# Kernel tuning notes

Hardware: AMD Instinct MI355X
Metric: run time of the kernel (lower is better)

## Reference

```python
import jax, jax.numpy as jnp
import numpy as np

MSA_DIM = 256
N_HEADS = 8
HEAD_DIM = MSA_DIM // N_HEADS
PAIR_DIM = 128
SCALE = 1.0 / float(np.sqrt(HEAD_DIM))


def setup_inputs() -> dict:
    key = jax.random.key(0)
    ks = jax.random.split(key, 7)
    B, S, L = 1, 128, 384
    return {
        "msa": jax.random.normal(ks[0], (B, S, L, MSA_DIM), dtype=jnp.float32),
        "pair": jax.random.normal(ks[1], (B, L, L, PAIR_DIM), dtype=jnp.float32),
        "Wq": jax.random.normal(ks[2], (MSA_DIM, MSA_DIM), dtype=jnp.float32) * 0.02,
        "Wk": jax.random.normal(ks[3], (MSA_DIM, MSA_DIM), dtype=jnp.float32) * 0.02,
        "Wv": jax.random.normal(ks[4], (MSA_DIM, MSA_DIM), dtype=jnp.float32) * 0.02,
        "Wo": jax.random.normal(ks[5], (MSA_DIM, MSA_DIM), dtype=jnp.float32) * 0.02,
        "Wpb": jax.random.normal(ks[6], (N_HEADS, PAIR_DIM), dtype=jnp.float32) * 0.02,
    }


def reference(msa, pair, Wq, Wk, Wv, Wo, Wpb):
    B, S, L, D = msa.shape
    H, hd = N_HEADS, HEAD_DIM
    # projections (nn.Linear: y = x @ W.T), split heads -> (B,S,H,L,hd)
    q = (msa @ Wq.T).reshape(B, S, L, H, hd)
    k = (msa @ Wk.T).reshape(B, S, L, H, hd)
    v = (msa @ Wv.T).reshape(B, S, L, H, hd)
    # NOTE: faithful to the original forward — pair_bias is computed but the
    # Triton kernel performs plain flash attention, so the bias is NOT added.
    _pair_bias = jnp.einsum('bijp,hp->bhij', pair, Wpb)  # dead code, as in source
    # attention logits per MSA row: (B,S,H,L,L)
    scores = jnp.einsum('bslhd,bsmhd->bshlm', q, k) * SCALE
    attn = jax.nn.softmax(scores, axis=-1)
    out = jnp.einsum('bshlm,bsmhd->bslhd', attn, v).reshape(B, S, L, D)
    return out @ Wo.T
```

## Files before the change

### kernel.cpp

```cpp
#include <hip/hip_runtime.h>
#include <stdint.h>

typedef unsigned short u16;
typedef __bf16 bf16x8 __attribute__((ext_vector_type(8)));
typedef short s16x4 __attribute__((ext_vector_type(4)));
typedef float f32x4 __attribute__((ext_vector_type(4)));

#define QKV_STRIDE 12288

__device__ __forceinline__ u16 f2bf(float x) {
    unsigned int u = __float_as_uint(x);
    u += 0x7fffu + ((u >> 16) & 1u);
    return (u16)(u >> 16);
}
__device__ __forceinline__ float bf2f(u16 h) {
    return __uint_as_float(((unsigned int)h) << 16);
}
__device__ __forceinline__ float tbf(float x) {
    return __uint_as_float(__float_as_uint(x) & 0xffff0000u);
}

static __device__ __forceinline__ f32x4 pv_mfma(s16x4 a, s16x4 b, f32x4 c) {
#if __has_builtin(__builtin_amdgcn_mfma_f32_16x16x16bf16_1k)
    return __builtin_amdgcn_mfma_f32_16x16x16bf16_1k(a, b, c, 0, 0, 0);
#else
    union { s16x4 h[2]; bf16x8 v; } ua, ub;
    s16x4 zz = {0, 0, 0, 0};
    ua.h[0] = a; ua.h[1] = zz;
    ub.h[0] = b; ub.h[1] = zz;
    return __builtin_amdgcn_mfma_f32_16x16x32_bf16(ua.v, ub.v, c, 0, 0, 0);
#endif
}

__global__ void convert_msa(const float* __restrict__ src, u16* __restrict__ dst) {
    int i = blockIdx.x * 256 + threadIdx.x;
    float4 v = ((const float4*)src)[i];
    ushort4 o;
    o.x = f2bf(v.x); o.y = f2bf(v.y); o.z = f2bf(v.z); o.w = f2bf(v.w);
    ((ushort4*)dst)[i] = o;
}

__global__ void pack_weights(const float* __restrict__ Wq, const float* __restrict__ Wk,
                             const float* __restrict__ Wv, const float* __restrict__ Wo,
                             u16* __restrict__ Wqkv, u16* __restrict__ Woh, u16* __restrict__ Wol) {
    int i = blockIdx.x * 256 + threadIdx.x;
    Wqkv[i]          = f2bf(Wq[i]);
    Wqkv[65536 + i]  = f2bf(Wk[i]);
    Wqkv[131072 + i] = f2bf(Wv[i]);
    float w = Wo[i];
    u16 hi = f2bf(w);
    Woh[i] = hi;
    Wol[i] = f2bf(w - bf2f(hi));
}

__launch_bounds__(256, 2)
__global__ void qkv_gemm(const u16* __restrict__ A, const u16* __restrict__ W,
                         u16* __restrict__ Qb, u16* __restrict__ Kb, u16* __restrict__ VTb) {
    __shared__ __align__(16) u16 As[128 * 32];
    __shared__ __align__(16) u16 Bs[128 * 32];
    const int tid = threadIdx.x;
    const int tm = blockIdx.x % 384, tn = blockIdx.x / 384;
    const bool trans = (tn < 4);
    const int lane = tid & 63, wave = tid >> 6;
    const int lm = lane & 15, lq = lane >> 4;
    const int wm = (wave >> 1) * 64, wn = (wave & 1) * 64;
    const float CEXPF = 0.17677669529663687f * 1.4426950408889634f;
    f32x4 acc[4][4] = {};

    const int ra = tid >> 2, ka = (tid & 3) << 3;
    const int rb = ra + 64;

    for (int k0 = 0; k0 < 256; k0 += 32) {
        *(uint4*)&As[ra * 32 + ka] = *(const uint4*)&A[(tm * 128 + ra) * 256 + k0 + ka];
        *(uint4*)&As[rb * 32 + ka] = *(const uint4*)&A[(tm * 128 + rb) * 256 + k0 + ka];
        *(uint4*)&Bs[ra * 32 + ka] = *(const uint4*)&W[(tn * 128 + ra) * 256 + k0 + ka];
        *(uint4*)&Bs[rb * 32 + ka] = *(const uint4*)&W[(tn * 128 + rb) * 256 + k0 + ka];
        __syncthreads();
        const u16* Xs = trans ? Bs : As;
        const u16* Ys = trans ? As : Bs;
        bf16x8 xf[4], yf[4];
        #pragma unroll
        for (int i = 0; i < 4; ++i)
            xf[i] = *(const bf16x8*)&Xs[(wm + i * 16 + lm) * 32 + lq * 8];
        #pragma unroll
        for (int j = 0; j < 4; ++j)
            yf[j] = *(const bf16x8*)&Ys[(wn + j * 16 + lm) * 32 + lq * 8];
        #pragma unroll
        for (int i = 0; i < 4; ++i)
            #pragma unroll
            for (int j = 0; j < 4; ++j)
                acc[i][j] = __builtin_amdgcn_mfma_f32_16x16x32_bf16(xf[i], yf[j], acc[i][j], 0, 0, 0);
        __syncthreads();
    }

    if (trans) {
        #pragma unroll
        for (int i = 0; i < 4; ++i) {
            int F0 = tn * 128 + wm + i * 16 + lq * 4;
            int which = F0 >> 8;
            int h = (F0 >> 5) & 7, d0 = F0 & 31;
            u16* dst = which ? Kb : Qb;
            float scale = which ? 1.0f : CEXPF;
            #pragma unroll
            for (int j = 0; j < 4; ++j) {
                int R = tm * 128 + wn + j * 16 + lm;
                int s = R / 384, l = R - s * 384;
                ushort4 o;
                o.x = f2bf(acc[i][j][0] * scale);
                o.y = f2bf(acc[i][j][1] * scale);
                o.z = f2bf(acc[i][j][2] * scale);
                o.w = f2bf(acc[i][j][3] * scale);
                *(ushort4*)&dst[((s * 8 + h) * 384 + l) * 32 + d0] = o;
            }
        }
    } else {
        #pragma unroll
        for (int j = 0; j < 4; ++j) {
            int F = tn * 128 + wn + j * 16 + lm;
            int h = (F >> 5) & 7, d = F & 31;
            #pragma unroll
            for (int i = 0; i < 4; ++i) {
                int R0 = tm * 128 + wm + i * 16 + lq * 4;
                int s = R0 / 384, l0 = R0 - s * 384;
                ushort4 o;
                o.x = f2bf(acc[i][j][0]);
                o.y = f2bf(acc[i][j][1]);
                o.z = f2bf(acc[i][j][2]);
                o.w = f2bf(acc[i][j][3]);
                *(ushort4*)&VTb[((s * 8 + h) * 32 + d) * 384 + l0] = o;
            }
        }
    }
}

__launch_bounds__(256, 3)
__global__ void msa_attention(const u16* __restrict__ Qb, const u16* __restrict__ Kb,
                              const u16* __restrict__ VTb,
                              u16* __restrict__ Ahi, u16* __restrict__ Alo) {
    __shared__ __align__(16) u16 Ks[384 * 32];
    __shared__ __align__(16) u16 Vt[32 * 392];
    const int tid = threadIdx.x;
    const int sh = blockIdx.x;
    const int s = sh >> 3, h = sh & 7;
    const u16* Qg = Qb + (size_t)sh * QKV_STRIDE;
    const u16* Kg = Kb + (size_t)sh * QKV_STRIDE;
    const u16* Vg = VTb + (size_t)sh * QKV_STRIDE;

    for (int i = tid; i < 1536; i += 256)
        *(uint4*)&Ks[i * 8] = *(const uint4*)&Kg[i * 8];
    for (int i = tid; i < 1536; i += 256) {
        int d = i / 48, c = i - d * 48;
        *(uint4*)&Vt[d * 392 + c * 8] = *(const uint4*)&Vg[d * 384 + c * 8];
    }

    const int lane = tid & 63, wave = tid >> 6;
    const int lm = lane & 15, lq = lane >> 4;

    bf16x8 aq[6];
    #pragma unroll
    for (int it = 0; it < 6; ++it)
        aq[it] = *(const bf16x8*)&Qg[((it * 4 + wave) * 16 + lm) * 32 + lq * 8];
    __syncthreads();

    f32x4 o[6][2] = {};
    float ls[6] = {0.f, 0.f, 0.f, 0.f, 0.f, 0.f};

    for (int n0 = 0; n0 < 384; n0 += 32) {
        bf16x8 kf0 = *(const bf16x8*)&Ks[(n0 + lm) * 32 + lq * 8];
        bf16x8 kf1 = *(const bf16x8*)&Ks[(n0 + 16 + lm) * 32 + lq * 8];
        s16x4 vf00 = *(const s16x4*)&Vt[lm * 392 + n0 + lq * 4];
        s16x4 vf01 = *(const s16x4*)&Vt[lm * 392 + n0 + 16 + lq * 4];
        s16x4 vf10 = *(const s16x4*)&Vt[(16 + lm) * 392 + n0 + lq * 4];
        s16x4 vf11 = *(const s16x4*)&Vt[(16 + lm) * 392 + n0 + 16 + lq * 4];
        #pragma unroll
        for (int it = 0; it < 6; ++it) {
            f32x4 z = {0.f, 0.f, 0.f, 0.f};
            f32x4 s0 = __builtin_amdgcn_mfma_f32_16x16x32_bf16(kf0, aq[it], z, 0, 0, 0);
            f32x4 s1 = __builtin_amdgcn_mfma_f32_16x16x32_bf16(kf1, aq[it], z, 0, 0, 0);
            float p0[4], p1[4];
            float a = 0.f;
            #pragma unroll
            for (int r = 0; r < 4; ++r) {
                p0[r] = __builtin_amdgcn_exp2f(s0[r]);
                p1[r] = __builtin_amdgcn_exp2f(s1[r]);
                a += tbf(p0[r]) + tbf(p1[r]);
            }
            ls[it] += a;
            union { s16x4 v; uint2 u; } pk0, pk1;
            pk0.u.x = __builtin_amdgcn_perm(__float_as_uint(p0[1]), __float_as_uint(p0[0]), 0x07060302u);
            pk0.u.y = __builtin_amdgcn_perm(__float_as_uint(p0[3]), __float_as_uint(p0[2]), 0x07060302u);
            pk1.u.x = __builtin_amdgcn_perm(__float_as_uint(p1[1]), __float_as_uint(p1[0]), 0x07060302u);
            pk1.u.y = __builtin_amdgcn_perm(__float_as_uint(p1[3]), __float_as_uint(p1[2]), 0x07060302u);
            o[it][0] = pv_mfma(vf00, pk0.v, o[it][0]);
            o[it][0] = pv_mfma(vf01, pk1.v, o[it][0]);
            o[it][1] = pv_mfma(vf10, pk0.v, o[it][1]);
            o[it][1] = pv_mfma(vf11, pk1.v, o[it][1]);
        }
    }

    #pragma unroll
    for (int it = 0; it < 6; ++it) {
        float L = ls[it];
        L += __shfl_xor(L, 16, 64);
        L += __shfl_xor(L, 32, 64);
        float inv = __builtin_amdgcn_rcpf(L);
        int l = (it * 4 + wave) * 16 + lm;
        int base = (s * 384 + l) * 256 + h * 32 + lq * 4;
        #pragma unroll
        for (int dt = 0; dt < 2; ++dt) {
            ushort4 oh, ol;
            float x0 = o[it][dt][0] * inv, x1 = o[it][dt][1] * inv;
            float x2 = o[it][dt][2] * inv, x3 = o[it][dt][3] * inv;
            oh.x = f2bf(x0); ol.x = f2bf(x0 - bf2f(oh.x));
            oh.y = f2bf(x1); ol.y = f2bf(x1 - bf2f(oh.y));
            oh.z = f2bf(x2); ol.z = f2bf(x2 - bf2f(oh.z));
            oh.w = f2bf(x3); ol.w = f2bf(x3 - bf2f(oh.w));
            *(ushort4*)&Ahi[base + dt * 16] = oh;
            *(ushort4*)&Alo[base + dt * 16] = ol;
        }
    }
}

__launch_bounds__(256, 2)
__global__ void out_gemm(const u16* __restrict__ Ahi, const u16* __restrict__ Alo,
                         const u16* __restrict__ Woh, const u16* __restrict__ Wol,
                         float* __restrict__ out) {
    __shared__ __align__(16) u16 Ah[128 * 32], Al[128 * 32], Bh[128 * 32], Bl[128 * 32];
    const int tid = threadIdx.x;
    const int tm = blockIdx.x % 384, tn = blockIdx.x / 384;
    const int lane = tid & 63, wave = tid >> 6;
    const int lm = lane & 15, lq = lane >> 4;
    const int wm = (wave >> 1) * 64, wn = (wave & 1) * 64;
    f32x4 acc[4][4] = {};

    const int ra = tid >> 2, ka = (tid & 3) << 3;
    const int rb = ra + 64;

    for (int k0 = 0; k0 < 256; k0 += 32) {
        *(uint4*)&Ah[ra * 32 + ka] = *(const uint4*)&Ahi[(tm * 128 + ra) * 256 + k0 + ka];
        *(uint4*)&Ah[rb * 32 + ka] = *(const uint4*)&Ahi[(tm * 128 + rb) * 256 + k0 + ka];
        *(uint4*)&Al[ra * 32 + ka] = *(const uint4*)&Alo[(tm * 128 + ra) * 256 + k0 + ka];
        *(uint4*)&Al[rb * 32 + ka] = *(const uint4*)&Alo[(tm * 128 + rb) * 256 + k0 + ka];
        *(uint4*)&Bh[ra * 32 + ka] = *(const uint4*)&Woh[(tn * 128 + ra) * 256 + k0 + ka];
        *(uint4*)&Bh[rb * 32 + ka] = *(const uint4*)&Woh[(tn * 128 + rb) * 256 + k0 + ka];
        *(uint4*)&Bl[ra * 32 + ka] = *(const uint4*)&Wol[(tn * 128 + ra) * 256 + k0 + ka];
        *(uint4*)&Bl[rb * 32 + ka] = *(const uint4*)&Wol[(tn * 128 + rb) * 256 + k0 + ka];
        __syncthreads();
        bf16x8 whf[4], wlf[4], ahf[4], alf[4];
        #pragma unroll
        for (int i = 0; i < 4; ++i) {
            whf[i] = *(const bf16x8*)&Bh[(wm + i * 16 + lm) * 32 + lq * 8];
            wlf[i] = *(const bf16x8*)&Bl[(wm + i * 16 + lm) * 32 + lq * 8];
        }
        #pragma unroll
        for (int j = 0; j < 4; ++j) {
            ahf[j] = *(const bf16x8*)&Ah[(wn + j * 16 + lm) * 32 + lq * 8];
            alf[j] = *(const bf16x8*)&Al[(wn + j * 16 + lm) * 32 + lq * 8];
        }
        #pragma unroll
        for (int i = 0; i < 4; ++i)
            #pragma unroll
            for (int j = 0; j < 4; ++j) {
                acc[i][j] = __builtin_amdgcn_mfma_f32_16x16x32_bf16(whf[i], alf[j], acc[i][j], 0, 0, 0);
                acc[i][j] = __builtin_amdgcn_mfma_f32_16x16x32_bf16(wlf[i], ahf[j], acc[i][j], 0, 0, 0);
                acc[i][j] = __builtin_amdgcn_mfma_f32_16x16x32_bf16(whf[i], ahf[j], acc[i][j], 0, 0, 0);
            }
        __syncthreads();
    }
    #pragma unroll
    for (int i = 0; i < 4; ++i) {
        int F0 = tn * 128 + wm + i * 16 + lq * 4;
        #pragma unroll
        for (int j = 0; j < 4; ++j) {
            int R = tm * 128 + wn + j * 16 + lm;
            *(f32x4*)&out[R * 256 + F0] = acc[i][j];
        }
    }
}

extern "C" void kernel_launch(void* const* d_in, const int* in_sizes, int n_in,
                              void* d_out, int out_size, void* d_ws, size_t ws_size,
                              hipStream_t stream) {
    const float* msa = (const float*)d_in[0];
    const float* Wq = (const float*)d_in[2];
    const float* Wk = (const float*)d_in[3];
    const float* Wv = (const float*)d_in[4];
    const float* Wo = (const float*)d_in[5];
    char* ws = (char*)d_ws;
    u16* msa_bf = (u16*)(ws + 0);
    u16* Qb     = (u16*)(ws + 25165824);
    u16* Kb     = (u16*)(ws + 50331648);
    u16* VTb    = (u16*)(ws + 75497472);
    u16* Ahi    = (u16*)(ws + 100663296);
    u16* Alo    = (u16*)(ws + 125829120);
    u16* Wqkv   = (u16*)(ws + 150994944);
    u16* Woh    = (u16*)(ws + 151388160);
    u16* Wol    = (u16*)(ws + 151519232);
    float* out  = (float*)d_out;

    hipLaunchKernelGGL(convert_msa, dim3(12288), dim3(256), 0, stream, msa, msa_bf);
    hipLaunchKernelGGL(pack_weights, dim3(256), dim3(256), 0, stream, Wq, Wk, Wv, Wo, Wqkv, Woh, Wol);
    hipLaunchKernelGGL(qkv_gemm, dim3(2304), dim3(256), 0, stream, msa_bf, Wqkv, Qb, Kb, VTb);
    hipLaunchKernelGGL(msa_attention, dim3(1024), dim3(256), 0, stream, Qb, Kb, VTb, Ahi, Alo);
    hipLaunchKernelGGL(out_gemm, dim3(768), dim3(256), 0, stream, Ahi, Alo, Woh, Wol, out);
}
```

Before: 283.6 us.

## Split attention over query thirds, use async LDS loads, fuse prep kernels

```diff
diff --git a/kernel.cpp b/kernel.cpp
--- a/kernel.cpp
+++ b/kernel.cpp
@@ -16,8 +16,11 @@
 __device__ __forceinline__ float bf2f(u16 h) {
     return __uint_as_float(((unsigned int)h) << 16);
 }
-__device__ __forceinline__ float tbf(float x) {
-    return __uint_as_float(__float_as_uint(x) & 0xffff0000u);
+
+__device__ __forceinline__ void async_copy16(const u16* g, u16* l) {
+    __builtin_amdgcn_global_load_lds(
+        (const __attribute__((address_space(1))) unsigned int*)g,
+        (__attribute__((address_space(3))) unsigned int*)l, 16, 0, 0);
 }
 
 static __device__ __forceinline__ f32x4 pv_mfma(s16x4 a, s16x4 b, f32x4 c) {
@@ -32,25 +35,28 @@
 #endif
 }
 
-__global__ void convert_msa(const float* __restrict__ src, u16* __restrict__ dst) {
-    int i = blockIdx.x * 256 + threadIdx.x;
-    float4 v = ((const float4*)src)[i];
-    ushort4 o;
-    o.x = f2bf(v.x); o.y = f2bf(v.y); o.z = f2bf(v.z); o.w = f2bf(v.w);
-    ((ushort4*)dst)[i] = o;
-}
-
-__global__ void pack_weights(const float* __restrict__ Wq, const float* __restrict__ Wk,
-                             const float* __restrict__ Wv, const float* __restrict__ Wo,
-                             u16* __restrict__ Wqkv, u16* __restrict__ Woh, u16* __restrict__ Wol) {
-    int i = blockIdx.x * 256 + threadIdx.x;
-    Wqkv[i]          = f2bf(Wq[i]);
-    Wqkv[65536 + i]  = f2bf(Wk[i]);
-    Wqkv[131072 + i] = f2bf(Wv[i]);
-    float w = Wo[i];
-    u16 hi = f2bf(w);
-    Woh[i] = hi;
-    Wol[i] = f2bf(w - bf2f(hi));
+__global__ void prep(const float* __restrict__ msa,
+                     const float* __restrict__ Wq, const float* __restrict__ Wk,
+                     const float* __restrict__ Wv, const float* __restrict__ Wo,
+                     u16* __restrict__ msa_bf, u16* __restrict__ Wqkv,
+                     u16* __restrict__ Woh, u16* __restrict__ Wol) {
+    int b = blockIdx.x;
+    if (b < 12288) {
+        int i = b * 256 + threadIdx.x;
+        float4 v = ((const float4*)msa)[i];
+        ushort4 o;
+        o.x = f2bf(v.x); o.y = f2bf(v.y); o.z = f2bf(v.z); o.w = f2bf(v.w);
+        ((ushort4*)msa_bf)[i] = o;
+    } else {
+        int i = (b - 12288) * 256 + threadIdx.x;
+        Wqkv[i]          = f2bf(Wq[i]);
+        Wqkv[65536 + i]  = f2bf(Wk[i]);
+        Wqkv[131072 + i] = f2bf(Wv[i]);
+        float w = Wo[i];
+        u16 hi = f2bf(w);
+        Woh[i] = hi;
+        Wol[i] = f2bf(w - bf2f(hi));
+    }
 }
 
 __launch_bounds__(256, 2)
@@ -67,14 +73,22 @@
     const float CEXPF = 0.17677669529663687f * 1.4426950408889634f;
     f32x4 acc[4][4] = {};
 
-    const int ra = tid >> 2, ka = (tid & 3) << 3;
-    const int rb = ra + 64;
+    const int srow = wave * 16 + (lane >> 2);
+    const int scol = (lane & 3) * 8;
+    u16* ldsA0 = &As[wave * 512 + lane * 8];
+    u16* ldsA1 = &As[2048 + wave * 512 + lane * 8];
+    u16* ldsB0 = &Bs[wave * 512 + lane * 8];
+    u16* ldsB1 = &Bs[2048 + wave * 512 + lane * 8];
+    const u16* gA0 = &A[(tm * 128 + srow) * 256 + scol];
+    const u16* gA1 = &A[(tm * 128 + 64 + srow) * 256 + scol];
+    const u16* gB0 = &W[(tn * 128 + srow) * 256 + scol];
+    const u16* gB1 = &W[(tn * 128 + 64 + srow) * 256 + scol];
 
     for (int k0 = 0; k0 < 256; k0 += 32) {
-        *(uint4*)&As[ra * 32 + ka] = *(const uint4*)&A[(tm * 128 + ra) * 256 + k0 + ka];
-        *(uint4*)&As[rb * 32 + ka] = *(const uint4*)&A[(tm * 128 + rb) * 256 + k0 + ka];
-        *(uint4*)&Bs[ra * 32 + ka] = *(const uint4*)&W[(tn * 128 + ra) * 256 + k0 + ka];
-        *(uint4*)&Bs[rb * 32 + ka] = *(const uint4*)&W[(tn * 128 + rb) * 256 + k0 + ka];
+        async_copy16(gA0 + k0, ldsA0);
+        async_copy16(gA1 + k0, ldsA1);
+        async_copy16(gB0 + k0, ldsB0);
+        async_copy16(gB1 + k0, ldsB1);
         __syncthreads();
         const u16* Xs = trans ? Bs : As;
         const u16* Ys = trans ? As : Bs;
@@ -133,21 +147,19 @@
     }
 }
 
-__launch_bounds__(256, 3)
+__launch_bounds__(256, 6)
 __global__ void msa_attention(const u16* __restrict__ Qb, const u16* __restrict__ Kb,
                               const u16* __restrict__ VTb,
                               u16* __restrict__ Ahi, u16* __restrict__ Alo) {
-    __shared__ __align__(16) u16 Ks[384 * 32];
     __shared__ __align__(16) u16 Vt[32 * 392];
     const int tid = threadIdx.x;
-    const int sh = blockIdx.x;
+    const int bid = blockIdx.x;
+    const int sh = bid / 3, lpart = bid - sh * 3;
     const int s = sh >> 3, h = sh & 7;
     const u16* Qg = Qb + (size_t)sh * QKV_STRIDE;
     const u16* Kg = Kb + (size_t)sh * QKV_STRIDE;
     const u16* Vg = VTb + (size_t)sh * QKV_STRIDE;
 
-    for (int i = tid; i < 1536; i += 256)
-        *(uint4*)&Ks[i * 8] = *(const uint4*)&Kg[i * 8];
     for (int i = tid; i < 1536; i += 256) {
         int d = i / 48, c = i - d * 48;
         *(uint4*)&Vt[d * 392 + c * 8] = *(const uint4*)&Vg[d * 384 + c * 8];
@@ -156,36 +168,36 @@
     const int lane = tid & 63, wave = tid >> 6;
     const int lm = lane & 15, lq = lane >> 4;
 
-    bf16x8 aq[6];
+    bf16x8 aq[2];
     #pragma unroll
-    for (int it = 0; it < 6; ++it)
-        aq[it] = *(const bf16x8*)&Qg[((it * 4 + wave) * 16 + lm) * 32 + lq * 8];
+    for (int it = 0; it < 2; ++it) {
+        int l = lpart * 128 + (wave * 2 + it) * 16 + lm;
+        aq[it] = *(const bf16x8*)&Qg[l * 32 + lq * 8];
+    }
     __syncthreads();
 
-    f32x4 o[6][2] = {};
-    float ls[6] = {0.f, 0.f, 0.f, 0.f, 0.f, 0.f};
+    f32x4 o[2][2] = {};
+    f32x4 lacc[2] = {};
+    const s16x4 ones = {(short)0x3F80, (short)0x3F80, (short)0x3F80, (short)0x3F80};
 
     for (int n0 = 0; n0 < 384; n0 += 32) {
-        bf16x8 kf0 = *(const bf16x8*)&Ks[(n0 + lm) * 32 + lq * 8];
-        bf16x8 kf1 = *(const bf16x8*)&Ks[(n0 + 16 + lm) * 32 + lq * 8];
+        bf16x8 kf0 = *(const bf16x8*)&Kg[(n0 + lm) * 32 + lq * 8];
+        bf16x8 kf1 = *(const bf16x8*)&Kg[(n0 + 16 + lm) * 32 + lq * 8];
         s16x4 vf00 = *(const s16x4*)&Vt[lm * 392 + n0 + lq * 4];
         s16x4 vf01 = *(const s16x4*)&Vt[lm * 392 + n0 + 16 + lq * 4];
         s16x4 vf10 = *(const s16x4*)&Vt[(16 + lm) * 392 + n0 + lq * 4];
         s16x4 vf11 = *(const s16x4*)&Vt[(16 + lm) * 392 + n0 + 16 + lq * 4];
         #pragma unroll
-        for (int it = 0; it < 6; ++it) {
+        for (int it = 0; it < 2; ++it) {
             f32x4 z = {0.f, 0.f, 0.f, 0.f};
             f32x4 s0 = __builtin_amdgcn_mfma_f32_16x16x32_bf16(kf0, aq[it], z, 0, 0, 0);
             f32x4 s1 = __builtin_amdgcn_mfma_f32_16x16x32_bf16(kf1, aq[it], z, 0, 0, 0);
             float p0[4], p1[4];
-            float a = 0.f;
             #pragma unroll
             for (int r = 0; r < 4; ++r) {
                 p0[r] = __builtin_amdgcn_exp2f(s0[r]);
                 p1[r] = __builtin_amdgcn_exp2f(s1[r]);
-                a += tbf(p0[r]) + tbf(p1[r]);
             }
-            ls[it] += a;
             union { s16x4 v; uint2 u; } pk0, pk1;
             pk0.u.x = __builtin_amdgcn_perm(__float_as_uint(p0[1]), __float_as_uint(p0[0]), 0x07060302u);
             pk0.u.y = __builtin_amdgcn_perm(__float_as_uint(p0[3]), __float_as_uint(p0[2]), 0x07060302u);
@@ -195,16 +207,15 @@
             o[it][0] = pv_mfma(vf01, pk1.v, o[it][0]);
             o[it][1] = pv_mfma(vf10, pk0.v, o[it][1]);
             o[it][1] = pv_mfma(vf11, pk1.v, o[it][1]);
+            lacc[it] = pv_mfma(ones, pk0.v, lacc[it]);
+            lacc[it] = pv_mfma(ones, pk1.v, lacc[it]);
         }
     }
 
     #pragma unroll
-    for (int it = 0; it < 6; ++it) {
-        float L = ls[it];
-        L += __shfl_xor(L, 16, 64);
-        L += __shfl_xor(L, 32, 64);
-        float inv = __builtin_amdgcn_rcpf(L);
-        int l = (it * 4 + wave) * 16 + lm;
+    for (int it = 0; it < 2; ++it) {
+        float inv = __builtin_amdgcn_rcpf(lacc[it][0]);
+        int l = lpart * 128 + (wave * 2 + it) * 16 + lm;
         int base = (s * 384 + l) * 256 + h * 32 + lq * 4;
         #pragma unroll
         for (int dt = 0; dt < 2; ++dt) {
@@ -233,18 +244,27 @@
     const int wm = (wave >> 1) * 64, wn = (wave & 1) * 64;
     f32x4 acc[4][4] = {};
 
-    const int ra = tid >> 2, ka = (tid & 3) << 3;
-    const int rb = ra + 64;
+    const int srow = wave * 16 + (lane >> 2);
+    const int scol = (lane & 3) * 8;
+    const int lo0 = wave * 512 + lane * 8, lo1 = 2048 + wave * 512 + lane * 8;
+    const u16* gAh0 = &Ahi[(tm * 128 + srow) * 256 + scol];
+    const u16* gAh1 = &Ahi[(tm * 128 + 64 + srow) * 256 + scol];
+    const u16* gAl0 = &Alo[(tm * 128 + srow) * 256 + scol];
+    const u16* gAl1 = &Alo[(tm * 128 + 64 + srow) * 256 + scol];
+    const u16* gBh0 = &Woh[(tn * 128 + srow) * 256 + scol];
+    const u16* gBh1 = &Woh[(tn * 128 + 64 + srow) * 256 + scol];
+    const u16* gBl0 = &Wol[(tn * 128 + srow) * 256 + scol];
+    const u16* gBl1 = &Wol[(tn * 128 + 64 + srow) * 256 + scol];
 
     for (int k0 = 0; k0 < 256; k0 += 32) {
-        *(uint4*)&Ah[ra * 32 + ka] = *(const uint4*)&Ahi[(tm * 128 + ra) * 256 + k0 + ka];
-        *(uint4*)&Ah[rb * 32 + ka] = *(const uint4*)&Ahi[(tm * 128 + rb) * 256 + k0 + ka];
-        *(uint4*)&Al[ra * 32 + ka] = *(const uint4*)&Alo[(tm * 128 + ra) * 256 + k0 + ka];
-        *(uint4*)&Al[rb * 32 + ka] = *(const uint4*)&Alo[(tm * 128 + rb) * 256 + k0 + ka];
-        *(uint4*)&Bh[ra * 32 + ka] = *(const uint4*)&Woh[(tn * 128 + ra) * 256 + k0 + ka];
-        *(uint4*)&Bh[rb * 32 + ka] = *(const uint4*)&Woh[(tn * 128 + rb) * 256 + k0 + ka];
-        *(uint4*)&Bl[ra * 32 + ka] = *(const uint4*)&Wol[(tn * 128 + ra) * 256 + k0 + ka];
-        *(uint4*)&Bl[rb * 32 + ka] = *(const uint4*)&Wol[(tn * 128 + rb) * 256 + k0 + ka];
+        async_copy16(gAh0 + k0, &Ah[lo0]);
+        async_copy16(gAh1 + k0, &Ah[lo1]);
+        async_copy16(gAl0 + k0, &Al[lo0]);
+        async_copy16(gAl1 + k0, &Al[lo1]);
+        async_copy16(gBh0 + k0, &Bh[lo0]);
+        async_copy16(gBh1 + k0, &Bh[lo1]);
+        async_copy16(gBl0 + k0, &Bl[lo0]);
+        async_copy16(gBl1 + k0, &Bl[lo1]);
         __syncthreads();
         bf16x8 whf[4], wlf[4], ahf[4], alf[4];
         #pragma unroll
@@ -298,9 +318,9 @@
     u16* Wol    = (u16*)(ws + 151519232);
     float* out  = (float*)d_out;
 
-    hipLaunchKernelGGL(convert_msa, dim3(12288), dim3(256), 0, stream, msa, msa_bf);
-    hipLaunchKernelGGL(pack_weights, dim3(256), dim3(256), 0, stream, Wq, Wk, Wv, Wo, Wqkv, Woh, Wol);
+    hipLaunchKernelGGL(prep, dim3(12544), dim3(256), 0, stream, msa, Wq, Wk, Wv, Wo,
+                       msa_bf, Wqkv, Woh, Wol);
     hipLaunchKernelGGL(qkv_gemm, dim3(2304), dim3(256), 0, stream, msa_bf, Wqkv, Qb, Kb, VTb);
-    hipLaunchKernelGGL(msa_attention, dim3(1024), dim3(256), 0, stream, Qb, Kb, VTb, Ahi, Alo);
+    hipLaunchKernelGGL(msa_attention, dim3(3072), dim3(256), 0, stream, Qb, Kb, VTb, Ahi, Alo);
     hipLaunchKernelGGL(out_gemm, dim3(768), dim3(256), 0, stream, Ahi, Alo, Woh, Wol, out);
 }
```

After: 264.8 us. 1.07x faster.
